# Kernel optimization log

Hardware: AMD Instinct MI355X
Metric: run time of the kernel (lower is better)

The kernel has to match this reference:

```python
import jax, jax.numpy as jnp
import numpy as np

H = 2048  # hidden_dim


def setup_inputs() -> dict:
    key = jax.random.key(0)
    ks = jax.random.split(key, 10)
    s = 1.0 / np.sqrt(H)
    x = jax.random.normal(ks[0], (4, 2048, H), dtype=jnp.float32)
    Wg = jax.random.uniform(ks[1], (2, H), jnp.float32, -s, s)          # gate weight [2, H]
    W0a = jax.random.uniform(ks[2], (2 * H, H), jnp.float32, -s, s)     # expert0 up
    b0a = jax.random.uniform(ks[3], (2 * H,), jnp.float32, -s, s)
    W0b = jax.random.uniform(ks[4], (H, 2 * H), jnp.float32, -s, s)     # expert0 down
    b0b = jax.random.uniform(ks[5], (H,), jnp.float32, -s, s)
    W1a = jax.random.uniform(ks[6], (2 * H, H), jnp.float32, -s, s)     # expert1 up
    b1a = jax.random.uniform(ks[7], (2 * H,), jnp.float32, -s, s)
    W1b = jax.random.uniform(ks[8], (H, 2 * H), jnp.float32, -s, s)     # expert1 down
    b1b = jax.random.uniform(ks[9], (H,), jnp.float32, -s, s)
    return {"x": x, "Wg": Wg, "W0a": W0a, "b0a": b0a, "W0b": W0b,
            "b0b": b0b, "W1a": W1a, "b1a": b1a, "W1b": W1b, "b1b": b1b}


def reference(x, Wg, W0a, b0a, W0b, b0b, W1a, b1a, W1b, b1b):
    # top-1 gating: softmax over 2 experts, then argmax
    scores = jax.nn.softmax(jnp.einsum('bsh,eh->bse', x, Wg), axis=-1)
    top_expert = jnp.argmax(scores, axis=-1)  # [B, S]
    # expert0: Linear -> GELU (exact, torch default) -> Linear
    h0 = jax.nn.gelu(jnp.einsum('bsh,fh->bsf', x, W0a) + b0a, approximate=False)
    out0 = jnp.einsum('bsf,hf->bsh', h0, W0b) + b0b
    # expert1: Linear -> ReLU -> Linear
    h1 = jax.nn.relu(jnp.einsum('bsh,fh->bsf', x, W1a) + b1a)
    out1 = jnp.einsum('bsf,hf->bsh', h1, W1b) + b1b
    mask0 = (top_expert == 0).astype(x.dtype)[..., None]
    return out0 * mask0 + out1 * (1.0 - mask0)
```

## Files before the change

kernel.cpp:

```cpp
#include <hip/hip_runtime.h>
#include <hip/hip_bf16.h>
#include <math.h>


#define HDIM   2048
#define TOKENS 8192
#define FDIM   4096

typedef __bf16 bf16x8 __attribute__((ext_vector_type(8)));
typedef __bf16 bf16x4 __attribute__((ext_vector_type(4)));
typedef float  f32x4  __attribute__((ext_vector_type(4)));

#define CNT_OFF  0
#define PERM_OFF 256
#define XG_OFF   65536
#define WA_OFF   33619968
#define WB_OFF   67174400
#define HB_OFF   100728832

typedef __attribute__((address_space(1))) const unsigned int as1_u32;
typedef __attribute__((address_space(3))) unsigned int       as3_u32;

__device__ __forceinline__ void gl2lds16(const void* g, void* l) {
    __builtin_amdgcn_global_load_lds((as1_u32*)g, (as3_u32*)l, 16, 0, 0);
}

__global__ void moe_gate_gather(const float* __restrict__ x, const float* __restrict__ Wg,
                                int* __restrict__ n0, int* __restrict__ n1,
                                int* __restrict__ perm, __bf16* __restrict__ Xg) {
    __shared__ int sel[4];
    __shared__ int pos[4];
    const int tid  = threadIdx.x;
    const int wid  = tid >> 6;
    const int lane = tid & 63;
    const int token = blockIdx.x * 4 + wid;
    const float* xr = x + (size_t)token * HDIM;

    float4 xv[8];
    double s0 = 0.0, s1 = 0.0;
#pragma unroll
    for (int j = 0; j < 8; j++) {
        const int idx = j * 256 + lane * 4;
        xv[j] = *reinterpret_cast<const float4*>(xr + idx);
        float4 g0 = *reinterpret_cast<const float4*>(Wg + idx);
        float4 g1 = *reinterpret_cast<const float4*>(Wg + HDIM + idx);
        s0 += (double)xv[j].x * g0.x + (double)xv[j].y * g0.y
            + (double)xv[j].z * g0.z + (double)xv[j].w * g0.w;
        s1 += (double)xv[j].x * g1.x + (double)xv[j].y * g1.y
            + (double)xv[j].z * g1.z + (double)xv[j].w * g1.w;
    }
#pragma unroll
    for (int off = 32; off > 0; off >>= 1) {
        s0 += __shfl_down(s0, off);
        s1 += __shfl_down(s1, off);
    }
    if (lane == 0) sel[wid] = (s1 > s0) ? 1 : 0;
    __syncthreads();
    if (tid == 0) {
        int c0 = (sel[0] == 0) + (sel[1] == 0) + (sel[2] == 0) + (sel[3] == 0);
        int p0 = c0 ? atomicAdd(n0, c0) : 0;
        int p1 = (c0 < 4) ? atomicAdd(n1, 4 - c0) : 0;
#pragma unroll
        for (int w = 0; w < 4; w++) {
            if (sel[w] == 0) pos[w] = p0++;
            else             pos[w] = TOKENS - 1 - (p1++);
        }
    }
    __syncthreads();
    const int dst = pos[wid];
    if (lane == 0) perm[dst] = token;
    __bf16* dr = Xg + (size_t)dst * HDIM;
#pragma unroll
    for (int j = 0; j < 8; j++) {
        const int idx = j * 256 + lane * 4;
        bf16x4 v;
        v[0] = (__bf16)xv[j].x; v[1] = (__bf16)xv[j].y;
        v[2] = (__bf16)xv[j].z; v[3] = (__bf16)xv[j].w;
        *reinterpret_cast<bf16x4*>(dr + idx) = v;
    }
}

__global__ void moe_cast_w(const float* __restrict__ W0a, const float* __restrict__ W1a,
                           const float* __restrict__ W0b, const float* __restrict__ W1b,
                           __bf16* __restrict__ Wa, __bf16* __restrict__ Wb) {
    const int slice = blockIdx.y;
    const float* src;
    __bf16* dst;
    const size_t MS = (size_t)FDIM * HDIM;
    if      (slice == 0) { src = W0a; dst = Wa; }
    else if (slice == 1) { src = W1a; dst = Wa + MS; }
    else if (slice == 2) { src = W0b; dst = Wb; }
    else                 { src = W1b; dst = Wb + MS; }
    const size_t idx = ((size_t)blockIdx.x * 256 + threadIdx.x) * 8;
    float4 a = *reinterpret_cast<const float4*>(src + idx);
    float4 b = *reinterpret_cast<const float4*>(src + idx + 4);
    bf16x8 v;
    v[0] = (__bf16)a.x; v[1] = (__bf16)a.y; v[2] = (__bf16)a.z; v[3] = (__bf16)a.w;
    v[4] = (__bf16)b.x; v[5] = (__bf16)b.y; v[6] = (__bf16)b.z; v[7] = (__bf16)b.w;
    *reinterpret_cast<bf16x8*>(dst + idx) = v;
}

template <int KDIM, int NDIM, bool DOWN>
__global__ void moe_gemm(const __bf16* __restrict__ A, const __bf16* __restrict__ Bw,
                         const float* __restrict__ bias0, const float* __restrict__ bias1,
                         __bf16* __restrict__ Hb, float* __restrict__ Out,
                         const int* __restrict__ n0_ptr, const int* __restrict__ perm) {
    const int e  = blockIdx.z;
    const int n0 = *n0_ptr;
    const int row_lo = e ? n0 : 0;
    const int row_hi = e ? TOKENS : n0;
    const int bm = blockIdx.y * 128;
    if (bm >= row_hi || bm + 128 <= row_lo) return;
    const int bn = blockIdx.x * 128;

    __shared__ __bf16 As[128 * 64];
    __shared__ __bf16 Bs[128 * 64];

    const int tid  = threadIdx.x;
    const int wid  = tid >> 6;
    const int lane = tid & 63;

    const __bf16* Be   = Bw + (size_t)e * NDIM * KDIM;
    const float*  bias = e ? bias1 : bias0;

    const int srow = wid * 32 + (lane >> 3);
    const int skol = (((lane & 7) ^ (lane >> 3)) * 8);
    const __bf16* gA = A  + (size_t)(bm + srow) * KDIM + skol;
    const __bf16* gB = Be + (size_t)(bn + srow) * KDIM + skol;
    __bf16* lA = &As[(wid * 32) * 64];
    __bf16* lB = &Bs[(wid * 32) * 64];

    const int wrow = (wid >> 1) * 64;
    const int wcol = (wid & 1) * 64;
    const int rm = lane & 15;
    const int g  = lane >> 4;
    const int rsw = rm & 7;

    f32x4 acc[4][4] = {};

    for (int kt = 0; kt < KDIM; kt += 64) {
#pragma unroll
        for (int c = 0; c < 4; c++) {
            gl2lds16(gA + (size_t)(c * 8) * KDIM + kt, lA + c * 8 * 64);
            gl2lds16(gB + (size_t)(c * 8) * KDIM + kt, lB + c * 8 * 64);
        }
        __syncthreads();

        bf16x8 aF[2][4], bF[2][4];
#pragma unroll
        for (int h = 0; h < 2; h++) {
            const int csw = ((h * 4 + g) ^ rsw) * 8;
#pragma unroll
            for (int i = 0; i < 4; i++) {
                aF[h][i] = *reinterpret_cast<const bf16x8*>(&As[(wrow + i * 16 + rm) * 64 + csw]);
                bF[h][i] = *reinterpret_cast<const bf16x8*>(&Bs[(wcol + i * 16 + rm) * 64 + csw]);
            }
        }
#pragma unroll
        for (int h = 0; h < 2; h++)
#pragma unroll
            for (int i = 0; i < 4; i++)
#pragma unroll
                for (int j = 0; j < 4; j++)
                    acc[i][j] = __builtin_amdgcn_mfma_f32_16x16x32_bf16(aF[h][i], bF[h][j], acc[i][j], 0, 0, 0);
        __syncthreads();
    }

    const int q4 = g * 4;
#pragma unroll
    for (int j = 0; j < 4; j++) {
        const int col = bn + wcol + j * 16 + rm;
        const float bv = bias[col];
#pragma unroll
        for (int i = 0; i < 4; i++) {
            const int rbase = bm + wrow + i * 16 + q4;
#pragma unroll
            for (int r = 0; r < 4; r++) {
                const int row = rbase + r;
                if (row >= row_lo && row < row_hi) {
                    float v = acc[i][j][r] + bv;
                    if (!DOWN) {
                        if (e == 0) v = 0.5f * v * (1.0f + erff(v * 0.70710678118654752f));
                        else        v = v > 0.0f ? v : 0.0f;
                        Hb[(size_t)row * NDIM + col] = (__bf16)v;
                    } else {
                        Out[(size_t)perm[row] * HDIM + col] = v;
                    }
                }
            }
        }
    }
}

extern "C" void kernel_launch(void* const* d_in, const int* in_sizes, int n_in,
                              void* d_out, int out_size, void* d_ws, size_t ws_size,
                              hipStream_t stream) {
    const float* x   = (const float*)d_in[0];
    const float* Wg  = (const float*)d_in[1];
    const float* W0a = (const float*)d_in[2];
    const float* b0a = (const float*)d_in[3];
    const float* W0b = (const float*)d_in[4];
    const float* b0b = (const float*)d_in[5];
    const float* W1a = (const float*)d_in[6];
    const float* b1a = (const float*)d_in[7];
    const float* W1b = (const float*)d_in[8];
    const float* b1b = (const float*)d_in[9];
    float* out = (float*)d_out;

    char* w = (char*)d_ws;
    int* n0   = (int*)(w + CNT_OFF);
    int* n1   = n0 + 1;
    int* perm = (int*)(w + PERM_OFF);
    __bf16* Xg = (__bf16*)(w + XG_OFF);
    __bf16* Wa = (__bf16*)(w + WA_OFF);
    __bf16* Wb = (__bf16*)(w + WB_OFF);
    __bf16* Hb = (__bf16*)(w + HB_OFF);

    (void)hipMemsetAsync(w, 0, 256, stream);
    moe_gate_gather<<<TOKENS / 4, 256, 0, stream>>>(x, Wg, n0, n1, perm, Xg);
    moe_cast_w<<<dim3(4096, 4), 256, 0, stream>>>(W0a, W1a, W0b, W1b, Wa, Wb);
    moe_gemm<HDIM, FDIM, false><<<dim3(FDIM / 128, TOKENS / 128, 2), 256, 0, stream>>>(
        Xg, Wa, b0a, b1a, Hb, nullptr, n0, perm);
    moe_gemm<FDIM, HDIM, true><<<dim3(HDIM / 128, TOKENS / 128, 2), 256, 0, stream>>>(
        Hb, Wb, b0b, b1b, nullptr, out, n0, perm);
}
```

Measured before the change: 603.7 us.

## Double-buffer GEMM LDS tiles with K=32 steps and fuse prep kernels

The GEMM main loop now uses two LDS buffers of 128x32 tiles and prefetches the next K-slice while MFMAs run on the current one. This leaves one barrier per iteration instead of two and hides global-to-LDS load latency. Separately, the gate/gather and weight-cast kernels are merged into a single launch to drop one kernel launch. In exchange, the K step is halved, so each iteration does fewer MFMAs per barrier. The swizzle is also reworked for the 32-wide tiles.

```diff
diff --git a/kernel.cpp b/kernel.cpp
--- a/kernel.cpp
+++ b/kernel.cpp
@@ -25,12 +25,35 @@
     __builtin_amdgcn_global_load_lds((as1_u32*)g, (as3_u32*)l, 16, 0, 0);
 }
 
-__global__ void moe_gate_gather(const float* __restrict__ x, const float* __restrict__ Wg,
-                                int* __restrict__ n0, int* __restrict__ n1,
-                                int* __restrict__ perm, __bf16* __restrict__ Xg) {
+__global__ void moe_prep(const float* __restrict__ x, const float* __restrict__ Wg,
+                         const float* __restrict__ W0a, const float* __restrict__ W1a,
+                         const float* __restrict__ W0b, const float* __restrict__ W1b,
+                         int* __restrict__ n0, int* __restrict__ n1,
+                         int* __restrict__ perm, __bf16* __restrict__ Xg,
+                         __bf16* __restrict__ Wa, __bf16* __restrict__ Wb) {
+    const int tid  = threadIdx.x;
+    if (blockIdx.x >= 2048) {
+        const int cb    = blockIdx.x - 2048;
+        const int slice = cb >> 12;
+        const int bx    = cb & 4095;
+        const float* src;
+        __bf16* dst;
+        const size_t MS = (size_t)FDIM * HDIM;
+        if      (slice == 0) { src = W0a; dst = Wa; }
+        else if (slice == 1) { src = W1a; dst = Wa + MS; }
+        else if (slice == 2) { src = W0b; dst = Wb; }
+        else                 { src = W1b; dst = Wb + MS; }
+        const size_t idx = ((size_t)bx * 256 + tid) * 8;
+        float4 a = *reinterpret_cast<const float4*>(src + idx);
+        float4 b = *reinterpret_cast<const float4*>(src + idx + 4);
+        bf16x8 v;
+        v[0] = (__bf16)a.x; v[1] = (__bf16)a.y; v[2] = (__bf16)a.z; v[3] = (__bf16)a.w;
+        v[4] = (__bf16)b.x; v[5] = (__bf16)b.y; v[6] = (__bf16)b.z; v[7] = (__bf16)b.w;
+        *reinterpret_cast<bf16x8*>(dst + idx) = v;
+        return;
+    }
     __shared__ int sel[4];
     __shared__ int pos[4];
-    const int tid  = threadIdx.x;
     const int wid  = tid >> 6;
     const int lane = tid & 63;
     const int token = blockIdx.x * 4 + wid;
@@ -78,26 +101,6 @@
         v[2] = (__bf16)xv[j].z; v[3] = (__bf16)xv[j].w;
         *reinterpret_cast<bf16x4*>(dr + idx) = v;
     }
-}
-
-__global__ void moe_cast_w(const float* __restrict__ W0a, const float* __restrict__ W1a,
-                           const float* __restrict__ W0b, const float* __restrict__ W1b,
-                           __bf16* __restrict__ Wa, __bf16* __restrict__ Wb) {
-    const int slice = blockIdx.y;
-    const float* src;
-    __bf16* dst;
-    const size_t MS = (size_t)FDIM * HDIM;
-    if      (slice == 0) { src = W0a; dst = Wa; }
-    else if (slice == 1) { src = W1a; dst = Wa + MS; }
-    else if (slice == 2) { src = W0b; dst = Wb; }
-    else                 { src = W1b; dst = Wb + MS; }
-    const size_t idx = ((size_t)blockIdx.x * 256 + threadIdx.x) * 8;
-    float4 a = *reinterpret_cast<const float4*>(src + idx);
-    float4 b = *reinterpret_cast<const float4*>(src + idx + 4);
-    bf16x8 v;
-    v[0] = (__bf16)a.x; v[1] = (__bf16)a.y; v[2] = (__bf16)a.z; v[3] = (__bf16)a.w;
-    v[4] = (__bf16)b.x; v[5] = (__bf16)b.y; v[6] = (__bf16)b.z; v[7] = (__bf16)b.w;
-    *reinterpret_cast<bf16x8*>(dst + idx) = v;
 }
 
 template <int KDIM, int NDIM, bool DOWN>
@@ -113,8 +116,8 @@
     if (bm >= row_hi || bm + 128 <= row_lo) return;
     const int bn = blockIdx.x * 128;
 
-    __shared__ __bf16 As[128 * 64];
-    __shared__ __bf16 Bs[128 * 64];
+    __shared__ __bf16 As[2][128 * 32];
+    __shared__ __bf16 Bs[2][128 * 32];
 
     const int tid  = threadIdx.x;
     const int wid  = tid >> 6;
@@ -123,47 +126,50 @@
     const __bf16* Be   = Bw + (size_t)e * NDIM * KDIM;
     const float*  bias = e ? bias1 : bias0;
 
-    const int srow = wid * 32 + (lane >> 3);
-    const int skol = (((lane & 7) ^ (lane >> 3)) * 8);
-    const __bf16* gA = A  + (size_t)(bm + srow) * KDIM + skol;
-    const __bf16* gB = Be + (size_t)(bn + srow) * KDIM + skol;
-    __bf16* lA = &As[(wid * 32) * 64];
-    __bf16* lB = &Bs[(wid * 32) * 64];
+    const int lr  = lane >> 2;
+    const int ssw = (((lane & 3) ^ ((lane >> 3) & 3)) * 8);
+    const __bf16* gA0 = A  + (size_t)(bm + wid * 32 + lr) * KDIM + ssw;
+    const __bf16* gA1 = gA0 + (size_t)16 * KDIM;
+    const __bf16* gB0 = Be + (size_t)(bn + wid * 32 + lr) * KDIM + ssw;
+    const __bf16* gB1 = gB0 + (size_t)16 * KDIM;
+    const int lbase0 = (wid * 32) * 32;
+    const int lbase1 = (wid * 32 + 16) * 32;
 
     const int wrow = (wid >> 1) * 64;
     const int wcol = (wid & 1) * 64;
     const int rm = lane & 15;
     const int g  = lane >> 4;
-    const int rsw = rm & 7;
+    const int csw = ((g ^ ((rm >> 1) & 3)) * 8);
 
     f32x4 acc[4][4] = {};
 
-    for (int kt = 0; kt < KDIM; kt += 64) {
-#pragma unroll
-        for (int c = 0; c < 4; c++) {
-            gl2lds16(gA + (size_t)(c * 8) * KDIM + kt, lA + c * 8 * 64);
-            gl2lds16(gB + (size_t)(c * 8) * KDIM + kt, lB + c * 8 * 64);
-        }
+    gl2lds16(gA0, &As[0][lbase0]);
+    gl2lds16(gA1, &As[0][lbase1]);
+    gl2lds16(gB0, &Bs[0][lbase0]);
+    gl2lds16(gB1, &Bs[0][lbase1]);
+
+    int p = 0;
+    for (int kt = 0; kt < KDIM; kt += 32) {
         __syncthreads();
-
-        bf16x8 aF[2][4], bF[2][4];
-#pragma unroll
-        for (int h = 0; h < 2; h++) {
-            const int csw = ((h * 4 + g) ^ rsw) * 8;
-#pragma unroll
-            for (int i = 0; i < 4; i++) {
-                aF[h][i] = *reinterpret_cast<const bf16x8*>(&As[(wrow + i * 16 + rm) * 64 + csw]);
-                bF[h][i] = *reinterpret_cast<const bf16x8*>(&Bs[(wcol + i * 16 + rm) * 64 + csw]);
-            }
-        }
-#pragma unroll
-        for (int h = 0; h < 2; h++)
-#pragma unroll
-            for (int i = 0; i < 4; i++)
-#pragma unroll
-                for (int j = 0; j < 4; j++)
-                    acc[i][j] = __builtin_amdgcn_mfma_f32_16x16x32_bf16(aF[h][i], bF[h][j], acc[i][j], 0, 0, 0);
-        __syncthreads();
+        if (kt + 32 < KDIM) {
+            const int q = p ^ 1;
+            gl2lds16(gA0 + kt + 32, &As[q][lbase0]);
+            gl2lds16(gA1 + kt + 32, &As[q][lbase1]);
+            gl2lds16(gB0 + kt + 32, &Bs[q][lbase0]);
+            gl2lds16(gB1 + kt + 32, &Bs[q][lbase1]);
+        }
+        bf16x8 aF[4], bF[4];
+#pragma unroll
+        for (int i = 0; i < 4; i++) {
+            aF[i] = *reinterpret_cast<const bf16x8*>(&As[p][(wrow + i * 16 + rm) * 32 + csw]);
+            bF[i] = *reinterpret_cast<const bf16x8*>(&Bs[p][(wcol + i * 16 + rm) * 32 + csw]);
+        }
+#pragma unroll
+        for (int i = 0; i < 4; i++)
+#pragma unroll
+            for (int j = 0; j < 4; j++)
+                acc[i][j] = __builtin_amdgcn_mfma_f32_16x16x32_bf16(aF[i], bF[j], acc[i][j], 0, 0, 0);
+        p ^= 1;
     }
 
     const int q4 = g * 4;
@@ -217,8 +223,8 @@
     __bf16* Hb = (__bf16*)(w + HB_OFF);
 
     (void)hipMemsetAsync(w, 0, 256, stream);
-    moe_gate_gather<<<TOKENS / 4, 256, 0, stream>>>(x, Wg, n0, n1, perm, Xg);
-    moe_cast_w<<<dim3(4096, 4), 256, 0, stream>>>(W0a, W1a, W0b, W1b, Wa, Wb);
+    moe_prep<<<2048 + 16384, 256, 0, stream>>>(x, Wg, W0a, W1a, W0b, W1b,
+                                               n0, n1, perm, Xg, Wa, Wb);
     moe_gemm<HDIM, FDIM, false><<<dim3(FDIM / 128, TOKENS / 128, 2), 256, 0, stream>>>(
         Xg, Wa, b0a, b1a, Hb, nullptr, n0, perm);
     moe_gemm<FDIM, HDIM, true><<<dim3(HDIM / 128, TOKENS / 128, 2), 256, 0, stream>>>(
```

New measurement: 679.0 us. +12.5%, slower.
